# Optimization experiments

Measured on AMD Instinct MI355X. Metric: run time of the kernel, lower is better.

Reference implementation:

```python
import jax, jax.numpy as jnp
import numpy as np

SPATIAL_DIM = 2
N_IN = 4096
N_OUT = 1024
C_IN = 32
C_OUT = 32
FILTER_SEQ = (64, 64)
BATCH = 16


def _grid(num_points):
    # replicates: meshgrid(indexing='xy') of linspace(0,1,n) per dim, dstack, view(-1, d)
    n = int(num_points ** (1.0 / SPATIAL_DIM))
    nodes = np.linspace(0.0, 1.0, n)
    X, Y = np.meshgrid(nodes, nodes, indexing='xy')
    return np.dstack((X, Y)).reshape(-1, SPATIAL_DIM)  # (n^2, 2)


def _cache():
    # replicates QuadConvLayer.cache(): bump-support sparsity pattern
    out_locs = _grid(N_OUT)               # (N_OUT, 2)
    in_nodes = _grid(N_IN)                # (N_IN, 2)
    locs = out_locs[:, None, :] - in_nodes[None, :, :]   # (N_OUT, N_IN, 2)
    bump_arg = np.linalg.norm(locs, axis=2) ** 4
    decay_param = (N_IN / 16.0) ** 2
    mask = bump_arg <= 1.0 / decay_param
    idx = np.argwhere(mask)               # (E, 2), row-major sorted like torch.nonzero
    eval_locs = locs[mask]                # (E, 2)
    return eval_locs.astype(np.float32), idx.astype(np.int64)


def setup_inputs() -> dict:
    key = jax.random.key(0)
    k_feat, k1, k2, k3 = jax.random.split(key, 4)
    eval_locs, eval_indices = _cache()
    # filter MLP G: Linear(2,64,bias=False) -> Sin -> Linear(64,64) -> Sin -> Linear(64, C_IN*C_OUT)
    d0, d1, d2, d3 = SPATIAL_DIM, FILTER_SEQ[0], FILTER_SEQ[1], C_IN * C_OUT
    W1 = jax.random.normal(k1, (d0, d1), jnp.float32) / np.sqrt(d0)
    W2 = jax.random.normal(k2, (d1, d2), jnp.float32) / np.sqrt(d1)
    W3 = jax.random.normal(k3, (d2, d3), jnp.float32) / np.sqrt(d2)
    features = jax.random.normal(k_feat, (BATCH, C_IN, N_IN), jnp.float32)
    return {
        "features": features,
        "W1": W1,
        "W2": W2,
        "W3": W3,
        "eval_locs": jnp.asarray(eval_locs),
        "eval_indices": jnp.asarray(eval_indices),
    }


def reference(features, W1, W2, W3, eval_locs, eval_indices):
    B = features.shape[0]
    E = eval_locs.shape[0]
    seg = eval_indices[:, 0]   # output point per edge (sorted)
    src = eval_indices[:, 1]   # input point per edge
    # filter MLP with Sin activations: (E, 2) -> (E, C_IN, C_OUT)
    h = jnp.sin(eval_locs @ W1)
    h = jnp.sin(h @ W2)
    filt = (h @ W3).reshape(E, C_IN, C_OUT)
    # gather features at source points: (B, C_IN, E)
    gathered = features[:, :, src]
    # faithful to torch: a raw reshape (NOT a transpose) of (B, C_IN, E) -> (B, E, C_IN)
    g = gathered.reshape(B, E, C_IN)
    vals = jnp.einsum('bni,nij->bnj', g, filt)   # (B, E, C_OUT)
    # faithful raw reshape (B, E, C_OUT) -> (B, C_OUT, E)
    vals = vals.reshape(B, C_OUT, E)
    # scatter-sum over edges into output points (segment_coo sum)
    integral = jnp.zeros((B, C_OUT, N_OUT), features.dtype).at[:, :, seg].add(vals)
    return integral
```

## Files before the change

kernel.cpp:

```cpp
#include <hip/hip_runtime.h>
#include <hip/hip_bf16.h>

typedef __bf16 bf16x4  __attribute__((ext_vector_type(4)));
typedef __bf16 bf16x8  __attribute__((ext_vector_type(8)));
typedef __bf16 bf16x16 __attribute__((ext_vector_type(16)));
typedef float  f32x4   __attribute__((ext_vector_type(4)));

#define N_IN   4096
#define N_OUT  1024
#define BATCH  16
#define ROWS   16

#define H1_STR   72
#define H2_STR   72
#define FT_JSTR  40
#define FTH_NSTR 648
#define G_STR    520
#define V_STR    520
#define GSTR2    1048
#define FB_FT_NSTR 1288
#define SEG_STR  34
#define WSLAB    2592
#define TILE_K   132

#define WS_W3T_OFF    0
#define WS_W2T_OFF    131072
#define WS_FEATT_OFF  139264
#define WS_NEED       4333568

__global__ void qc_zero_kernel(float* __restrict__ out, int n4) {
    int i = blockIdx.x * blockDim.x + threadIdx.x;
    if (i < n4) ((float4*)out)[i] = make_float4(0.f, 0.f, 0.f, 0.f);
}

__global__ void qc_prep_kernel(const float* __restrict__ w3, const float* __restrict__ w2,
                               __bf16* __restrict__ w3t, __bf16* __restrict__ w2t) {
    int gid = blockIdx.x * blockDim.x + threadIdx.x;
    if (gid < 65536) {
        int k = gid & 63, col = gid >> 6;
        w3t[gid] = (__bf16)w3[k * 1024 + col];
    } else {
        int j = gid - 65536;
        int k = j & 63, col = j >> 6;
        w2t[j] = (__bf16)w2[k * 64 + col];
    }
}

__global__ void qc_prep2_kernel(const float* __restrict__ w3, const float* __restrict__ w2,
                                const float* __restrict__ feat,
                                float* __restrict__ out,
                                __bf16* __restrict__ w3t, __bf16* __restrict__ w2t,
                                __bf16* __restrict__ featT) {
    int bid = blockIdx.x, tid = threadIdx.x;
    if (bid < 512) {
        int c    = bid >> 4;
        int src  = (bid & 15) * 256 + tid;
        bf16x16 v;
        #pragma unroll
        for (int b = 0; b < 16; ++b)
            v[b] = (__bf16)feat[(b * 32 + c) * N_IN + src];
        __bf16* p = &featT[((size_t)c * N_IN + src) * 16];
        *(bf16x8*)p       = *(bf16x8*)&v;
        *(bf16x8*)(p + 8) = *((bf16x8*)&v + 1);
    } else if (bid < 528) {
        __shared__ float tile[64][65];
        const int colbase = (bid - 512) * 64;
        #pragma unroll
        for (int it = 0; it < 16; ++it) {
            int k = it * 4 + (tid >> 6);
            int c = tid & 63;
            tile[k][c] = w3[k * 1024 + colbase + c];
        }
        __syncthreads();
        int cc = tid >> 2;
        int k0 = (tid & 3) * 16;
        bf16x8 o0, o1;
        #pragma unroll
        for (int z = 0; z < 8; ++z) {
            o0[z] = (__bf16)tile[k0 + z][cc];
            o1[z] = (__bf16)tile[k0 + 8 + z][cc];
        }
        __bf16* wp = &w3t[(colbase + cc) * 64 + k0];
        *(bf16x8*)wp       = o0;
        *(bf16x8*)(wp + 8) = o1;
    } else if (bid == 528) {
        #pragma unroll
        for (int z = 0; z < 16; ++z) {
            int j = tid * 16 + z;
            w2t[j] = (__bf16)w2[(j & 63) * 64 + (j >> 6)];
        }
    } else {
        int i = (bid - 529) * 256 + tid;
        ((float4*)out)[i] = make_float4(0.f, 0.f, 0.f, 0.f);
    }
}

__global__ __launch_bounds__(512, 2)
void qc_fused32_kernel(const __bf16* __restrict__ featT,
                       const float* __restrict__ w1,
                       const float* __restrict__ locs,
                       const int*   __restrict__ eidx,
                       const __bf16* __restrict__ w2t,
                       const __bf16* __restrict__ w3t,
                       float* __restrict__ out,
                       int E)
{
    __shared__ __align__(16) unsigned char region1[41472];
    __shared__ __align__(16) unsigned char region2[9216];
    __shared__ unsigned short seg_s[32 * SEG_STR];

    __bf16* gb   = (__bf16*)region1;
    __bf16* ftv  = (__bf16*)region1;
    __bf16* vals = (__bf16*)region1;

    __bf16* h1b  = (__bf16*)region2;
    __bf16* h2b  = (__bf16*)(region2 + 9216/2);
    float*  tile = (float*)region2;

    const int tid  = threadIdx.x;
    const int lane = tid & 63;
    const int wv   = tid >> 6;
    const int ml   = lane & 15;
    const int q    = lane >> 4;
    const int n0   = blockIdx.x * 32;
    const int t0   = n0 * 32;
    const int ch0  = t0 / E;
    const int m0   = t0 - ch0 * E;

    const int tlb = wv * 128 + lane;
    bf16x16 gvv[2];
    int sgv[2];
    #pragma unroll
    for (int h = 0; h < 2; ++h) {
        int tl = tlb + h * 64;
        int mm = m0 + tl;
        int cc = ch0 + (mm >= E);
        if (mm >= E) mm -= E;
        int2 p = ((const int2*)eidx)[mm];
        sgv[h] = p.x;
        int ccc = cc < 32 ? cc : 31;
        bf16x16 g = *(const bf16x16*)&featT[((size_t)ccc * N_IN + p.y) * 16];
        if (cc >= 32) {
            #pragma unroll
            for (int z = 0; z < 16; ++z) g[z] = (__bf16)0.f;
        }
        gvv[h] = g;
    }
    const int rg = (wv >> 2) * 16;
    const int cw = (wv & 3) * 16;
    const bf16x8 bw0 = *(const bf16x8*)&w2t[(cw + ml) * 64 + q * 8];
    const bf16x8 bw1 = *(const bf16x8*)&w2t[(cw + ml) * 64 + 32 + q * 8];

    {
        const int r  = tid >> 4;
        const int j0 = (tid & 15) * 4;
        float lx = 0.f, ly = 0.f;
        int n = n0 + r;
        if (n < E) { lx = locs[n * 2]; ly = locs[n * 2 + 1]; }
        float4 wa = *(const float4*)&w1[j0];
        float4 wb = *(const float4*)&w1[64 + j0];
        __bf16* hp = &h1b[r * H1_STR + j0];
        hp[0] = (__bf16)__sinf(lx * wa.x + ly * wb.x);
        hp[1] = (__bf16)__sinf(lx * wa.y + ly * wb.y);
        hp[2] = (__bf16)__sinf(lx * wa.z + ly * wb.z);
        hp[3] = (__bf16)__sinf(lx * wa.w + ly * wb.w);
    }
    __syncthreads();

    {
        bf16x8 a0 = *(const bf16x8*)&h1b[(rg + ml) * H1_STR + q * 8];
        bf16x8 a1 = *(const bf16x8*)&h1b[(rg + ml) * H1_STR + 32 + q * 8];
        f32x4 c = {0.f, 0.f, 0.f, 0.f};
        c = __builtin_amdgcn_mfma_f32_16x16x32_bf16(a0, bw0, c, 0, 0, 0);
        c = __builtin_amdgcn_mfma_f32_16x16x32_bf16(a1, bw1, c, 0, 0, 0);
        #pragma unroll
        for (int g_ = 0; g_ < 4; ++g_)
            h2b[(rg + q * 4 + g_) * H2_STR + cw + ml] = (__bf16)__sinf(c[g_]);
    }

    #pragma unroll
    for (int b = 0; b < 16; ++b) {
        gb[b * GSTR2 + tlb]      = gvv[0][b];
        gb[b * GSTR2 + tlb + 64] = gvv[1][b];
    }
    seg_s[(tlb >> 5) * SEG_STR + (tlb & 31)] = (unsigned short)sgv[0];
    {
        int tl1 = tlb + 64;
        seg_s[(tl1 >> 5) * SEG_STR + (tl1 & 31)] = (unsigned short)sgv[1];
    }
    bf16x8 ag[4];
    #pragma unroll
    for (int rr = 0; rr < 4; ++rr)
        ag[rr] = *(const bf16x8*)&gb[ml * GSTR2 + (wv * 4 + rr) * 32 + q * 8];
    __syncthreads();

    bf16x8 ha00 = *(const bf16x8*)&h2b[ml * H2_STR + q * 8];
    bf16x8 ha01 = *(const bf16x8*)&h2b[ml * H2_STR + 32 + q * 8];
    bf16x8 ha10 = *(const bf16x8*)&h2b[(16 + ml) * H2_STR + q * 8];
    bf16x8 ha11 = *(const bf16x8*)&h2b[(16 + ml) * H2_STR + 32 + q * 8];

    f32x4 c0[4], c1[4];

    {
        f32x4 accA[4], accB[4];
        #pragma unroll
        for (int tt = 0; tt < 4; ++tt) {
            int i_  = wv * 4 + tt;
            int col = i_ * 32 + ml;
            const __bf16* wp = &w3t[col * 64 + q * 8];
            bf16x8 b0 = *(const bf16x8*)wp;
            bf16x8 b1 = *(const bf16x8*)(wp + 32);
            f32x4 cA = {0.f, 0.f, 0.f, 0.f};
            f32x4 cB = {0.f, 0.f, 0.f, 0.f};
            cA = __builtin_amdgcn_mfma_f32_16x16x32_bf16(ha00, b0, cA, 0, 0, 0);
            cA = __builtin_amdgcn_mfma_f32_16x16x32_bf16(ha01, b1, cA, 0, 0, 0);
            cB = __builtin_amdgcn_mfma_f32_16x16x32_bf16(ha10, b0, cB, 0, 0, 0);
            cB = __builtin_amdgcn_mfma_f32_16x16x32_bf16(ha11, b1, cB, 0, 0, 0);
            accA[tt] = cA; accB[tt] = cB;
        }
        #pragma unroll
        for (int g_ = 0; g_ < 4; ++g_) {
            bf16x4 pa, pb;
            #pragma unroll
            for (int tt = 0; tt < 4; ++tt) {
                pa[tt] = (__bf16)accA[tt][g_];
                pb[tt] = (__bf16)accB[tt][g_];
            }
            *(bf16x4*)&ftv[(q * 4 + g_) * FTH_NSTR + ml * FT_JSTR + wv * 4]        = pa;
            *(bf16x4*)&ftv[(16 + q * 4 + g_) * FTH_NSTR + ml * FT_JSTR + wv * 4]   = pb;
        }
    }
    __syncthreads();

    #pragma unroll
    for (int z = 0; z < 5; ++z) {
        int i = tid + z * 512;
        if (i < 16 * TILE_K) tile[i] = 0.f;
    }

    {
        bf16x8 f[4];
        #pragma unroll
        for (int rr = 0; rr < 4; ++rr)
            f[rr] = *(const bf16x8*)&ftv[(wv * 4 + rr) * FTH_NSTR + ml * FT_JSTR + q * 8];
        #pragma unroll
        for (int rr = 0; rr < 4; ++rr) {
            f32x4 z = {0.f, 0.f, 0.f, 0.f};
            c0[rr] = __builtin_amdgcn_mfma_f32_16x16x32_bf16(ag[rr], f[rr], z, 0, 0, 0);
        }
    }
    __syncthreads();

    {
        f32x4 accA[4], accB[4];
        #pragma unroll
        for (int tt = 0; tt < 4; ++tt) {
            int i_  = wv * 4 + tt;
            int col = i_ * 32 + 16 + ml;
            const __bf16* wp = &w3t[col * 64 + q * 8];
            bf16x8 b0 = *(const bf16x8*)wp;
            bf16x8 b1 = *(const bf16x8*)(wp + 32);
            f32x4 cA = {0.f, 0.f, 0.f, 0.f};
            f32x4 cB = {0.f, 0.f, 0.f, 0.f};
            cA = __builtin_amdgcn_mfma_f32_16x16x32_bf16(ha00, b0, cA, 0, 0, 0);
            cA = __builtin_amdgcn_mfma_f32_16x16x32_bf16(ha01, b1, cA, 0, 0, 0);
            cB = __builtin_amdgcn_mfma_f32_16x16x32_bf16(ha10, b0, cB, 0, 0, 0);
            cB = __builtin_amdgcn_mfma_f32_16x16x32_bf16(ha11, b1, cB, 0, 0, 0);
            accA[tt] = cA; accB[tt] = cB;
        }
        #pragma unroll
        for (int g_ = 0; g_ < 4; ++g_) {
            bf16x4 pa, pb;
            #pragma unroll
            for (int tt = 0; tt < 4; ++tt) {
                pa[tt] = (__bf16)accA[tt][g_];
                pb[tt] = (__bf16)accB[tt][g_];
            }
            *(bf16x4*)&ftv[(q * 4 + g_) * FTH_NSTR + ml * FT_JSTR + wv * 4]        = pa;
            *(bf16x4*)&ftv[(16 + q * 4 + g_) * FTH_NSTR + ml * FT_JSTR + wv * 4]   = pb;
        }
    }
    __syncthreads();

    const int seg0 = (int)seg_s[0];
    const int segL = (int)seg_s[31 * SEG_STR + 31];
    const int tlw  = E - m0;
    const bool wrap = (tlw < 1024);
    int OFF = 0, NK;
    if (wrap) {
        int tw = tlw - 1;
        OFF = (int)seg_s[(tw >> 5) * SEG_STR + (tw & 31)] - seg0 + 1;
        NK  = OFF + segL + 1;
    } else {
        NK = segL - seg0 + 1;
    }

    {
        bf16x8 f1[4];
        #pragma unroll
        for (int rr = 0; rr < 4; ++rr)
            f1[rr] = *(const bf16x8*)&ftv[(wv * 4 + rr) * FTH_NSTR + ml * FT_JSTR + q * 8];
        #pragma unroll
        for (int rr = 0; rr < 4; ++rr) {
            f32x4 z = {0.f, 0.f, 0.f, 0.f};
            c1[rr] = __builtin_amdgcn_mfma_f32_16x16x32_bf16(ag[rr], f1[rr], z, 0, 0, 0);
        }
        __bf16* vslab = &vals[wv * WSLAB];
        #pragma unroll
        for (int rr = 0; rr < 4; ++rr) {
            __bf16* vp = &vslab[rr * FTH_NSTR];
            #pragma unroll
            for (int g_ = 0; g_ < 4; ++g_) {
                int b = q * 4 + g_;
                vp[b * FT_JSTR + ml]      = (__bf16)c0[rr][g_];
                vp[b * FT_JSTR + 16 + ml] = (__bf16)c1[rr][g_];
            }
        }

        const int q2 = lane >> 4;
        const int b  = lane & 15;
        const int w  = wv * 4 + q2;
        const __bf16* vp = &vslab[q2 * FTH_NSTR + b * FT_JSTR];
        bf16x8 v0 = *(const bf16x8*)(vp);
        bf16x8 v1 = *(const bf16x8*)(vp + 8);
        bf16x8 v2 = *(const bf16x8*)(vp + 16);
        bf16x8 v3 = *(const bf16x8*)(vp + 24);
        float vv[32];
        #pragma unroll
        for (int j = 0; j < 8; ++j) {
            vv[j]      = (float)v0[j];
            vv[8 + j]  = (float)v1[j];
            vv[16 + j] = (float)v2[j];
            vv[24 + j] = (float)v3[j];
        }

        int mwin = m0 + (w << 5);
        int cb   = ch0;
        if (mwin >= E) { mwin -= E; ++cb; }
        int jcross = E - mwin;

        if (NK <= TILE_K) {
            const int NEG = -0x40000000;
            int io0 = (cb < 32) ? ((cb == ch0) ? -seg0 : OFF) : NEG;
            int io1 = (cb + 1 < 32) ? OFF : NEG;
            int key_prev = -1;
            float acc = 0.f;
            #pragma unroll
            for (int j = 0; j < 32; ++j) {
                int io = (j < jcross) ? io0 : io1;
                if (io != NEG) {
                    int key = io + (int)seg_s[w * SEG_STR + j];
                    if (key != key_prev) {
                        if (key_prev >= 0) atomicAdd(&tile[b * TILE_K + key_prev], acc);
                        key_prev = key;
                        acc = vv[j];
                    } else {
                        acc += vv[j];
                    }
                }
            }
            if (key_prev >= 0) atomicAdd(&tile[b * TILE_K + key_prev], acc);
        } else {
            int base0 = (cb < 32)     ? ((b << 15) | (cb << 10))       : -1;
            int base1 = (cb + 1 < 32) ? ((b << 15) | ((cb + 1) << 10)) : -1;
            int key_prev = -1;
            float acc = 0.f;
            #pragma unroll
            for (int j = 0; j < 32; ++j) {
                int basej = (j < jcross) ? base0 : base1;
                if (basej >= 0) {
                    int key = basej + (int)seg_s[w * SEG_STR + j];
                    if (key != key_prev) {
                        if (key_prev >= 0) atomicAdd(&out[key_prev], acc);
                        key_prev = key;
                        acc = vv[j];
                    } else {
                        acc += vv[j];
                    }
                }
            }
            if (key_prev >= 0) atomicAdd(&out[key_prev], acc);
        }
    }

    if (NK <= TILE_K) {
        __syncthreads();

        int total = NK * 16;
        for (int t = tid; t < total; t += 512) {
            int bb = t / NK;
            int i  = t - bb * NK;
            int cbx, sg;
            if (wrap && i >= OFF) { cbx = ch0 + 1; sg = i - OFF; }
            else                  { cbx = ch0;     sg = seg0 + i; }
            if (cbx < 32) {
                float v = tile[bb * TILE_K + i];
                int o = (bb << 15) | (cbx << 10) | sg;
                bool bnd = (i == 0) || (i == NK - 1) ||
                           (wrap && (i == OFF - 1 || i == OFF));
                if (bnd) atomicAdd(&out[o], v);
                else     out[o] = v;
            }
        }
    }
}

__global__ __launch_bounds__(256, 2)
void qc_main_kernel(const float* __restrict__ feat,
                    const float* __restrict__ w1,
                    const float* __restrict__ w2,
                    const float* __restrict__ locs,
                    const int*   __restrict__ eidx,
                    const __bf16* __restrict__ w3t,
                    float* __restrict__ out,
                    int E)
{
    __shared__ __align__(16) __bf16 h1b[ROWS * H1_STR];
    __shared__ __align__(16) __bf16 h2b[ROWS * H2_STR];
    __shared__ __align__(16) __bf16 ftv[ROWS * FB_FT_NSTR];
    __shared__ __align__(16) __bf16 gb [BATCH * G_STR];
    __shared__ unsigned short seg_s[512];
    __shared__ unsigned short src_s[512];

    const int tid = threadIdx.x;
    const int n0  = blockIdx.x * ROWS;
    const int t0  = n0 * 32;
    const int ch0 = t0 / E;
    const int m0  = t0 - ch0 * E;

    {
        const int r  = tid >> 4;
        const int j0 = (tid & 15) * 4;
        float lx = 0.f, ly = 0.f;
        int n = n0 + r;
        if (n < E) { lx = locs[n * 2]; ly = locs[n * 2 + 1]; }
        float4 wa = *(const float4*)&w1[j0];
        float4 wb = *(const float4*)&w1[64 + j0];
        __bf16* h = &h1b[r * H1_STR + j0];
        h[0] = (__bf16)__sinf(lx * wa.x + ly * wb.x);
        h[1] = (__bf16)__sinf(lx * wa.y + ly * wb.y);
        h[2] = (__bf16)__sinf(lx * wa.z + ly * wb.z);
        h[3] = (__bf16)__sinf(lx * wa.w + ly * wb.w);
    }
    for (int tl = tid; tl < 512; tl += 256) {
        int mm = m0 + tl; if (mm >= E) mm -= E;
        seg_s[tl] = (unsigned short)eidx[mm * 2];
        src_s[tl] = (unsigned short)eidx[mm * 2 + 1];
    }
    __syncthreads();

    {
        const int r  = tid >> 4;
        const int j0 = (tid & 15) * 4;
        float a0 = 0.f, a1 = 0.f, a2 = 0.f, a3 = 0.f;
        const __bf16* h1r = &h1b[r * H1_STR];
        #pragma unroll 8
        for (int k = 0; k < 64; ++k) {
            float h = (float)h1r[k];
            float4 w = *(const float4*)&w2[k * 64 + j0];
            a0 += h * w.x; a1 += h * w.y; a2 += h * w.z; a3 += h * w.w;
        }
        __bf16* h = &h2b[r * H2_STR + j0];
        h[0] = (__bf16)__sinf(a0);
        h[1] = (__bf16)__sinf(a1);
        h[2] = (__bf16)__sinf(a2);
        h[3] = (__bf16)__sinf(a3);
    }
    #pragma unroll 4
    for (int it = 0; it < 32; ++it) {
        int idx = it * 256 + tid;
        int b   = idx >> 9;
        int tl  = idx & 511;
        int mm  = m0 + tl;
        int cc  = ch0 + (mm >= E);
        if (mm >= E) mm -= E;
        float v = 0.f;
        if (cc < 32) v = feat[(b * 32 + cc) * N_IN + (int)src_s[tl]];
        gb[b * G_STR + tl] = (__bf16)v;
    }
    __syncthreads();

    const int lane = tid & 63;
    const int wv   = tid >> 6;
    const int ml   = lane & 15;
    const int q    = lane >> 4;

    {
        bf16x8 a0 = *(const bf16x8*)&h2b[ml * H2_STR + q * 8];
        bf16x8 a1 = *(const bf16x8*)&h2b[ml * H2_STR + 32 + q * 8];
        #pragma unroll
        for (int t = 0; t < 16; ++t) {
            int col = wv * 256 + t * 16 + ml;
            const __bf16* wp = &w3t[col * 64 + q * 8];
            bf16x8 b0 = *(const bf16x8*)wp;
            bf16x8 b1 = *(const bf16x8*)(wp + 32);
            f32x4 c = {0.f, 0.f, 0.f, 0.f};
            c = __builtin_amdgcn_mfma_f32_16x16x32_bf16(a0, b0, c, 0, 0, 0);
            c = __builtin_amdgcn_mfma_f32_16x16x32_bf16(a1, b1, c, 0, 0, 0);
            int i_ = col >> 5, j_ = col & 31;
            __bf16* fp = &ftv[j_ * FT_JSTR + i_];
            fp[(q * 4 + 0) * FB_FT_NSTR] = (__bf16)c[0];
            fp[(q * 4 + 1) * FB_FT_NSTR] = (__bf16)c[1];
            fp[(q * 4 + 2) * FB_FT_NSTR] = (__bf16)c[2];
            fp[(q * 4 + 3) * FB_FT_NSTR] = (__bf16)c[3];
        }
    }
    __syncthreads();

    {
        bf16x8 ag[4], f0[4], f1[4];
        #pragma unroll
        for (int rr = 0; rr < 4; ++rr) {
            int r = wv * 4 + rr;
            ag[rr] = *(const bf16x8*)&gb[ml * G_STR + r * 32 + q * 8];
            f0[rr] = *(const bf16x8*)&ftv[r * FB_FT_NSTR + ml        * FT_JSTR + q * 8];
            f1[rr] = *(const bf16x8*)&ftv[r * FB_FT_NSTR + (16 + ml) * FT_JSTR + q * 8];
        }
        __syncthreads();
        __bf16* valsb = ftv;
        #pragma unroll
        for (int rr = 0; rr < 4; ++rr) {
            int r = wv * 4 + rr;
            f32x4 c0 = {0.f, 0.f, 0.f, 0.f};
            f32x4 c1 = {0.f, 0.f, 0.f, 0.f};
            c0 = __builtin_amdgcn_mfma_f32_16x16x32_bf16(ag[rr], f0[rr], c0, 0, 0, 0);
            c1 = __builtin_amdgcn_mfma_f32_16x16x32_bf16(ag[rr], f1[rr], c1, 0, 0, 0);
            __bf16* vp = &valsb[r * 32];
            #pragma unroll
            for (int g_ = 0; g_ < 4; ++g_) {
                int b = q * 4 + g_;
                vp[b * V_STR + ml]      = (__bf16)c0[g_];
                vp[b * V_STR + 16 + ml] = (__bf16)c1[g_];
            }
        }
    }
    __syncthreads();

    {
        const __bf16* valsb = ftv;
        const int b = tid >> 4;
        const int r = tid & 15;
        const __bf16* vp = &valsb[b * V_STR + r * 32];
        bf16x8 v0 = *(const bf16x8*)(vp);
        bf16x8 v1 = *(const bf16x8*)(vp + 8);
        bf16x8 v2 = *(const bf16x8*)(vp + 16);
        bf16x8 v3 = *(const bf16x8*)(vp + 24);
        float vv[32];
        #pragma unroll
        for (int j = 0; j < 8; ++j) {
            vv[j]      = (float)v0[j];
            vv[8 + j]  = (float)v1[j];
            vv[16 + j] = (float)v2[j];
            vv[24 + j] = (float)v3[j];
        }
        const int tl0 = r * 32;
        int key_prev = -1;
        float acc = 0.f;
        #pragma unroll
        for (int j = 0; j < 32; ++j) {
            int mm = m0 + tl0 + j;
            int cc = ch0 + (mm >= E);
            if (mm >= E) mm -= E;
            if (cc < 32) {
                int o   = (int)seg_s[tl0 + j];
                int key = ((b * 32 + cc) << 10) | o;
                if (key != key_prev) {
                    if (key_prev >= 0) atomicAdd(&out[key_prev], acc);
                    key_prev = key;
                    acc = vv[j];
                } else {
                    acc += vv[j];
                }
            }
        }
        if (key_prev >= 0) atomicAdd(&out[key_prev], acc);
    }
}

extern "C" void kernel_launch(void* const* d_in, const int* in_sizes, int n_in,
                              void* d_out, int out_size, void* d_ws, size_t ws_size,
                              hipStream_t stream)
{
    (void)n_in;
    const float* feat = (const float*)d_in[0];
    const float* w1   = (const float*)d_in[1];
    const float* w2   = (const float*)d_in[2];
    const float* w3   = (const float*)d_in[3];
    const float* locs = (const float*)d_in[4];
    const int*   eidx = (const int*)d_in[5];
    float* out  = (float*)d_out;

    const int E = in_sizes[4] / 2;
    if (E <= 0) return;

    __bf16* w3t   = (__bf16*)((char*)d_ws + WS_W3T_OFF);
    __bf16* w2t   = (__bf16*)((char*)d_ws + WS_W2T_OFF);
    __bf16* featT = (__bf16*)((char*)d_ws + WS_FEATT_OFF);

    if (ws_size >= (size_t)WS_NEED) {
        int nblocks = (E + 31) / 32;
        qc_prep2_kernel<<<1041, 256, 0, stream>>>(w3, w2, feat, out, w3t, w2t, featT);
        qc_fused32_kernel<<<nblocks, 512, 0, stream>>>(featT, w1, locs, eidx, w2t, w3t, out, E);
    } else {
        int n4 = out_size / 4;
        int nblocks = (E + ROWS - 1) / ROWS;
        qc_zero_kernel<<<(n4 + 255) / 256, 256, 0, stream>>>(out, n4);
        qc_prep_kernel<<<272, 256, 0, stream>>>(w3, w2, w3t, w2t);
        qc_main_kernel<<<nblocks, 256, 0, stream>>>(feat, w1, w2, locs, eidx, w3t, out, E);
    }
}
```

Before: 121.9 us.

## Halve fused kernel tile to 16 edges per 256-thread block for occupancy

The fused filter-MLP/gather/contract/scatter kernel now handles 16 edges per block with 4 waves instead of 32 edges with 8 waves, which halves the shared-memory footprint and raises the launch-bounds occupancy target to 6 blocks per CU. The W3 filter stage now computes one 16-row MFMA tile per wave over 8 column groups and writes packed bf16x8 values. The intent is more resident blocks for better latency hiding and finer load balance. In exchange, each W3 fragment loaded from global memory is reused over 16 rows instead of 32, and there are twice as many blocks doing scatter atomics over the output.

Result: slower. 137.0 us (+12.3%).

```diff
diff --git a/kernel.cpp b/kernel.cpp
--- a/kernel.cpp
+++ b/kernel.cpp
@@ -17,11 +17,10 @@
 #define FTH_NSTR 648
 #define G_STR    520
 #define V_STR    520
-#define GSTR2    1048
 #define FB_FT_NSTR 1288
 #define SEG_STR  34
 #define WSLAB    2592
-#define TILE_K   132
+#define TILE_K   80
 
 #define WS_W3T_OFF    0
 #define WS_W2T_OFF    131072
@@ -95,8 +94,8 @@
     }
 }
 
-__global__ __launch_bounds__(512, 2)
-void qc_fused32_kernel(const __bf16* __restrict__ featT,
+__global__ __launch_bounds__(256, 6)
+void qc_fused16_kernel(const __bf16* __restrict__ featT,
                        const float* __restrict__ w1,
                        const float* __restrict__ locs,
                        const int*   __restrict__ eidx,
@@ -105,16 +104,16 @@
                        float* __restrict__ out,
                        int E)
 {
-    __shared__ __align__(16) unsigned char region1[41472];
-    __shared__ __align__(16) unsigned char region2[9216];
-    __shared__ unsigned short seg_s[32 * SEG_STR];
+    __shared__ __align__(16) unsigned char region1[20736];
+    __shared__ __align__(16) unsigned char region2[5120];
+    __shared__ unsigned short seg_s[16 * SEG_STR];
 
     __bf16* gb   = (__bf16*)region1;
     __bf16* ftv  = (__bf16*)region1;
     __bf16* vals = (__bf16*)region1;
 
     __bf16* h1b  = (__bf16*)region2;
-    __bf16* h2b  = (__bf16*)(region2 + 9216/2);
+    __bf16* h2b  = (__bf16*)(region2 + 2304);
     float*  tile = (float*)region2;
 
     const int tid  = threadIdx.x;
@@ -122,7 +121,7 @@
     const int wv   = tid >> 6;
     const int ml   = lane & 15;
     const int q    = lane >> 4;
-    const int n0   = blockIdx.x * 32;
+    const int n0   = blockIdx.x * 16;
     const int t0   = n0 * 32;
     const int ch0  = t0 / E;
     const int m0   = t0 - ch0 * E;
@@ -146,8 +145,7 @@
         }
         gvv[h] = g;
     }
-    const int rg = (wv >> 2) * 16;
-    const int cw = (wv & 3) * 16;
+    const int cw = wv * 16;
     const bf16x8 bw0 = *(const bf16x8*)&w2t[(cw + ml) * 64 + q * 8];
     const bf16x8 bw1 = *(const bf16x8*)&w2t[(cw + ml) * 64 + 32 + q * 8];
 
@@ -168,20 +166,20 @@
     __syncthreads();
 
     {
-        bf16x8 a0 = *(const bf16x8*)&h1b[(rg + ml) * H1_STR + q * 8];
-        bf16x8 a1 = *(const bf16x8*)&h1b[(rg + ml) * H1_STR + 32 + q * 8];
+        bf16x8 a0 = *(const bf16x8*)&h1b[ml * H1_STR + q * 8];
+        bf16x8 a1 = *(const bf16x8*)&h1b[ml * H1_STR + 32 + q * 8];
         f32x4 c = {0.f, 0.f, 0.f, 0.f};
         c = __builtin_amdgcn_mfma_f32_16x16x32_bf16(a0, bw0, c, 0, 0, 0);
         c = __builtin_amdgcn_mfma_f32_16x16x32_bf16(a1, bw1, c, 0, 0, 0);
         #pragma unroll
         for (int g_ = 0; g_ < 4; ++g_)
-            h2b[(rg + q * 4 + g_) * H2_STR + cw + ml] = (__bf16)__sinf(c[g_]);
+            h2b[(q * 4 + g_) * H2_STR + cw + ml] = (__bf16)__sinf(c[g_]);
     }
 
     #pragma unroll
     for (int b = 0; b < 16; ++b) {
-        gb[b * GSTR2 + tlb]      = gvv[0][b];
-        gb[b * GSTR2 + tlb + 64] = gvv[1][b];
+        gb[b * G_STR + tlb]      = gvv[0][b];
+        gb[b * G_STR + tlb + 64] = gvv[1][b];
     }
     seg_s[(tlb >> 5) * SEG_STR + (tlb & 31)] = (unsigned short)sgv[0];
     {
@@ -191,50 +189,37 @@
     bf16x8 ag[4];
     #pragma unroll
     for (int rr = 0; rr < 4; ++rr)
-        ag[rr] = *(const bf16x8*)&gb[ml * GSTR2 + (wv * 4 + rr) * 32 + q * 8];
+        ag[rr] = *(const bf16x8*)&gb[ml * G_STR + (wv * 4 + rr) * 32 + q * 8];
     __syncthreads();
 
     bf16x8 ha00 = *(const bf16x8*)&h2b[ml * H2_STR + q * 8];
     bf16x8 ha01 = *(const bf16x8*)&h2b[ml * H2_STR + 32 + q * 8];
-    bf16x8 ha10 = *(const bf16x8*)&h2b[(16 + ml) * H2_STR + q * 8];
-    bf16x8 ha11 = *(const bf16x8*)&h2b[(16 + ml) * H2_STR + 32 + q * 8];
 
     f32x4 c0[4], c1[4];
 
     {
-        f32x4 accA[4], accB[4];
-        #pragma unroll
-        for (int tt = 0; tt < 4; ++tt) {
-            int i_  = wv * 4 + tt;
-            int col = i_ * 32 + ml;
+        bf16x8 pa[4];
+        #pragma unroll
+        for (int tt = 0; tt < 8; ++tt) {
+            int col = (wv * 8 + tt) * 32 + ml;
             const __bf16* wp = &w3t[col * 64 + q * 8];
             bf16x8 b0 = *(const bf16x8*)wp;
             bf16x8 b1 = *(const bf16x8*)(wp + 32);
             f32x4 cA = {0.f, 0.f, 0.f, 0.f};
-            f32x4 cB = {0.f, 0.f, 0.f, 0.f};
             cA = __builtin_amdgcn_mfma_f32_16x16x32_bf16(ha00, b0, cA, 0, 0, 0);
             cA = __builtin_amdgcn_mfma_f32_16x16x32_bf16(ha01, b1, cA, 0, 0, 0);
-            cB = __builtin_amdgcn_mfma_f32_16x16x32_bf16(ha10, b0, cB, 0, 0, 0);
-            cB = __builtin_amdgcn_mfma_f32_16x16x32_bf16(ha11, b1, cB, 0, 0, 0);
-            accA[tt] = cA; accB[tt] = cB;
-        }
-        #pragma unroll
-        for (int g_ = 0; g_ < 4; ++g_) {
-            bf16x4 pa, pb;
-            #pragma unroll
-            for (int tt = 0; tt < 4; ++tt) {
-                pa[tt] = (__bf16)accA[tt][g_];
-                pb[tt] = (__bf16)accB[tt][g_];
-            }
-            *(bf16x4*)&ftv[(q * 4 + g_) * FTH_NSTR + ml * FT_JSTR + wv * 4]        = pa;
-            *(bf16x4*)&ftv[(16 + q * 4 + g_) * FTH_NSTR + ml * FT_JSTR + wv * 4]   = pb;
-        }
+            #pragma unroll
+            for (int g_ = 0; g_ < 4; ++g_) pa[g_][tt] = (__bf16)cA[g_];
+        }
+        #pragma unroll
+        for (int g_ = 0; g_ < 4; ++g_)
+            *(bf16x8*)&ftv[(q * 4 + g_) * FTH_NSTR + ml * FT_JSTR + wv * 8] = pa[g_];
     }
     __syncthreads();
 
     #pragma unroll
     for (int z = 0; z < 5; ++z) {
-        int i = tid + z * 512;
+        int i = tid + z * 256;
         if (i < 16 * TILE_K) tile[i] = 0.f;
     }
 
@@ -252,40 +237,29 @@
     __syncthreads();
 
     {
-        f32x4 accA[4], accB[4];
-        #pragma unroll
-        for (int tt = 0; tt < 4; ++tt) {
-            int i_  = wv * 4 + tt;
-            int col = i_ * 32 + 16 + ml;
+        bf16x8 pa[4];
+        #pragma unroll
+        for (int tt = 0; tt < 8; ++tt) {
+            int col = (wv * 8 + tt) * 32 + 16 + ml;
             const __bf16* wp = &w3t[col * 64 + q * 8];
             bf16x8 b0 = *(const bf16x8*)wp;
             bf16x8 b1 = *(const bf16x8*)(wp + 32);
             f32x4 cA = {0.f, 0.f, 0.f, 0.f};
-            f32x4 cB = {0.f, 0.f, 0.f, 0.f};
             cA = __builtin_amdgcn_mfma_f32_16x16x32_bf16(ha00, b0, cA, 0, 0, 0);
             cA = __builtin_amdgcn_mfma_f32_16x16x32_bf16(ha01, b1, cA, 0, 0, 0);
-            cB = __builtin_amdgcn_mfma_f32_16x16x32_bf16(ha10, b0, cB, 0, 0, 0);
-            cB = __builtin_amdgcn_mfma_f32_16x16x32_bf16(ha11, b1, cB, 0, 0, 0);
-            accA[tt] = cA; accB[tt] = cB;
-        }
-        #pragma unroll
-        for (int g_ = 0; g_ < 4; ++g_) {
-            bf16x4 pa, pb;
-            #pragma unroll
-            for (int tt = 0; tt < 4; ++tt) {
-                pa[tt] = (__bf16)accA[tt][g_];
-                pb[tt] = (__bf16)accB[tt][g_];
-            }
-            *(bf16x4*)&ftv[(q * 4 + g_) * FTH_NSTR + ml * FT_JSTR + wv * 4]        = pa;
-            *(bf16x4*)&ftv[(16 + q * 4 + g_) * FTH_NSTR + ml * FT_JSTR + wv * 4]   = pb;
-        }
+            #pragma unroll
+            for (int g_ = 0; g_ < 4; ++g_) pa[g_][tt] = (__bf16)cA[g_];
+        }
+        #pragma unroll
+        for (int g_ = 0; g_ < 4; ++g_)
+            *(bf16x8*)&ftv[(q * 4 + g_) * FTH_NSTR + ml * FT_JSTR + wv * 8] = pa[g_];
     }
     __syncthreads();
 
     const int seg0 = (int)seg_s[0];
-    const int segL = (int)seg_s[31 * SEG_STR + 31];
+    const int segL = (int)seg_s[15 * SEG_STR + 31];
     const int tlw  = E - m0;
-    const bool wrap = (tlw < 1024);
+    const bool wrap = (tlw < 512);
     int OFF = 0, NK;
     if (wrap) {
         int tw = tlw - 1;
@@ -387,7 +361,7 @@
         __syncthreads();
 
         int total = NK * 16;
-        for (int t = tid; t < total; t += 512) {
+        for (int t = tid; t < total; t += 256) {
             int bb = t / NK;
             int i  = t - bb * NK;
             int cbx, sg;
@@ -418,7 +392,7 @@
     __shared__ __align__(16) __bf16 h1b[ROWS * H1_STR];
     __shared__ __align__(16) __bf16 h2b[ROWS * H2_STR];
     __shared__ __align__(16) __bf16 ftv[ROWS * FB_FT_NSTR];
-    __shared__ __align__(16) __bf16 gb [BATCH * G_STR];
+    __shared__ __align__(16) __bf16 gb [BATCH * V_STR];
     __shared__ unsigned short seg_s[512];
     __shared__ unsigned short src_s[512];
 
@@ -476,7 +450,7 @@
         if (mm >= E) mm -= E;
         float v = 0.f;
         if (cc < 32) v = feat[(b * 32 + cc) * N_IN + (int)src_s[tl]];
-        gb[b * G_STR + tl] = (__bf16)v;
+        gb[b * V_STR + tl] = (__bf16)v;
     }
     __syncthreads();
 
@@ -512,7 +486,7 @@
         #pragma unroll
         for (int rr = 0; rr < 4; ++rr) {
             int r = wv * 4 + rr;
-            ag[rr] = *(const bf16x8*)&gb[ml * G_STR + r * 32 + q * 8];
+            ag[rr] = *(const bf16x8*)&gb[ml * V_STR + r * 32 + q * 8];
             f0[rr] = *(const bf16x8*)&ftv[r * FB_FT_NSTR + ml        * FT_JSTR + q * 8];
             f1[rr] = *(const bf16x8*)&ftv[r * FB_FT_NSTR + (16 + ml) * FT_JSTR + q * 8];
         }
@@ -598,9 +572,9 @@
     __bf16* featT = (__bf16*)((char*)d_ws + WS_FEATT_OFF);
 
     if (ws_size >= (size_t)WS_NEED) {
-        int nblocks = (E + 31) / 32;
+        int nblocks = (E + 15) / 16;
         qc_prep2_kernel<<<1041, 256, 0, stream>>>(w3, w2, feat, out, w3t, w2t, featT);
-        qc_fused32_kernel<<<nblocks, 512, 0, stream>>>(featT, w1, locs, eidx, w2t, w3t, out, E);
+        qc_fused16_kernel<<<nblocks, 256, 0, stream>>>(featT, w1, locs, eidx, w2t, w3t, out, E);
     } else {
         int n4 = out_size / 4;
         int nblocks = (E + ROWS - 1) / ROWS;
```
